# Kernel optimization log

Hardware: AMD Instinct MI355X
Metric: run time of the kernel (lower is better)

Reference implementation:

```python
import jax, jax.numpy as jnp
import numpy as np

D_MODEL = 1024
NUM_HEADS = 16
D_K = D_MODEL // NUM_HEADS
THETA = 10000.0


def setup_inputs() -> dict:
    key = jax.random.key(0)
    ks = jax.random.split(key, 5)
    b, s = 4, 1024
    std = 1.0 / np.sqrt(D_MODEL)
    x = jax.random.normal(ks[0], (b, s, D_MODEL), dtype=jnp.float32)
    token_positions = jnp.tile(jnp.arange(s, dtype=jnp.int64)[None, :], (b, 1))
    Wq = jax.random.truncated_normal(ks[1], -3.0, 3.0, (D_MODEL, D_MODEL), jnp.float32) * std
    Wk = jax.random.truncated_normal(ks[2], -3.0, 3.0, (D_MODEL, D_MODEL), jnp.float32) * std
    Wv = jax.random.truncated_normal(ks[3], -3.0, 3.0, (D_MODEL, D_MODEL), jnp.float32) * std
    Wo = jax.random.truncated_normal(ks[4], -3.0, 3.0, (D_MODEL, D_MODEL), jnp.float32) * std
    return {"x": x, "token_positions": token_positions,
            "Wq": Wq, "Wk": Wk, "Wv": Wv, "Wo": Wo}


def _apply_rope(x):
    # x: [b, h, s, d_k]; source uses row index i (ignores token_positions)
    s, d = x.shape[-2], x.shape[-1]
    pos = jnp.arange(s, dtype=jnp.float32)                      # [s]
    kidx = jnp.arange(0, d, 2, dtype=jnp.float32)               # [d/2]
    ang = pos[:, None] / (THETA ** (kidx / d))                  # [s, d/2]
    cos, sin = jnp.cos(ang), jnp.sin(ang)
    x_even, x_odd = x[..., 0::2], x[..., 1::2]                  # [b,h,s,d/2]
    out_even = x_even * cos - x_odd * sin
    out_odd = x_even * sin + x_odd * cos
    return jnp.stack([out_even, out_odd], axis=-1).reshape(x.shape)


def reference(x, token_positions, Wq, Wk, Wv, Wo):
    b, s, _ = x.shape
    # Linear: einsum '... din, dout din -> ... dout'  => x @ W.T
    q = jnp.einsum('bsd,ed->bse', x, Wq)
    k = jnp.einsum('bsd,ed->bse', x, Wk)
    v = jnp.einsum('bsd,ed->bse', x, Wv)
    # split heads -> [b, h, s, d_k]
    def split(t):
        return t.reshape(b, s, NUM_HEADS, D_K).transpose(0, 2, 1, 3)
    q, k, v = split(q), split(k), split(v)
    q = _apply_rope(q)
    k = _apply_rope(k)
    scores = jnp.einsum('bhqd,bhkd->bhqk', q, k) / np.sqrt(D_K)
    causal = jnp.tril(jnp.ones((s, s), dtype=bool))
    scores = jnp.where(causal, scores, -jnp.inf)
    attn = jax.nn.softmax(scores, axis=-1)
    out = jnp.einsum('bhqk,bhkd->bhqd', attn, v)
    out = out.transpose(0, 2, 1, 3).reshape(b, s, D_MODEL)
    return jnp.einsum('bsd,ed->bse', out, Wo)
```

## Files before the change

kernel.cpp:

```cpp
#include <hip/hip_runtime.h>

typedef __attribute__((ext_vector_type(8))) short short8;
typedef __attribute__((ext_vector_type(8))) __bf16 bf16x8;
typedef __attribute__((ext_vector_type(4))) float f32x4;
typedef __attribute__((ext_vector_type(4))) float float4v;
typedef __attribute__((ext_vector_type(4))) unsigned short ushort4v;
typedef __attribute__((ext_vector_type(2))) unsigned uint2v;
typedef __attribute__((ext_vector_type(4))) unsigned uint4v;

#define AS1 __attribute__((address_space(1)))
#define AS3 __attribute__((address_space(3)))

#define BATCH 4
#define SEQ 1024
#define DM 1024
#define NH 16
#define DKH 64
#define MROWS (BATCH * SEQ)
#define N3 (3 * DM)

static __device__ __forceinline__ unsigned short f2bf(float f) {
  unsigned u = __builtin_bit_cast(unsigned, f);
  u += 0x7FFFu + ((u >> 16) & 1u);
  return (unsigned short)(u >> 16);
}
static __device__ __forceinline__ float bf2f(unsigned short h) {
  return __builtin_bit_cast(float, ((unsigned)h) << 16);
}
static __device__ __forceinline__ unsigned cvt_pk_bf16(float lo, float hi) {
  unsigned r;
  asm("v_cvt_pk_bf16_f32 %0, %1, %2" : "=v"(r) : "v"(lo), "v"(hi));
  return r;
}
static __device__ __forceinline__ f32x4 mfma16(short8 a, short8 b, f32x4 c) {
  return __builtin_amdgcn_mfma_f32_16x16x32_bf16(
      __builtin_bit_cast(bf16x8, a), __builtin_bit_cast(bf16x8, b), c, 0, 0, 0);
}

__global__ __launch_bounds__(256) void convert_kernel(
    const float* __restrict__ x, const float* __restrict__ wq,
    const float* __restrict__ wk, const float* __restrict__ wv,
    const float* __restrict__ wo, unsigned short* __restrict__ xb,
    unsigned short* __restrict__ wqkv, unsigned short* __restrict__ wob) {
  size_t i4 = ((size_t)blockIdx.x * 256 + threadIdx.x) * 4;
  const size_t SZX = (size_t)MROWS * DM;
  const size_t SZW = (size_t)DM * DM;
  const float* src;
  unsigned short* dst;
  size_t off;
  if (i4 < SZX) {
    src = x; dst = xb; off = i4;
  } else if (i4 < SZX + SZW) {
    src = wq; dst = wqkv; off = i4 - SZX;
  } else if (i4 < SZX + 2 * SZW) {
    src = wk; dst = wqkv + SZW; off = i4 - SZX - SZW;
  } else if (i4 < SZX + 3 * SZW) {
    src = wv; dst = wqkv + 2 * SZW; off = i4 - SZX - 2 * SZW;
  } else {
    src = wo; dst = wob; off = i4 - SZX - 3 * SZW;
  }
  float4v v = *(const float4v*)(src + off);
  uint2v o;
  o.x = cvt_pk_bf16(v.x, v.y);
  o.y = cvt_pk_bf16(v.z, v.w);
  *(uint2v*)(dst + off) = o;
}

static __device__ __forceinline__ void store_c(float* p, float v) { *p = v; }
static __device__ __forceinline__ void store_c(unsigned short* p, float v) { *p = f2bf(v); }

template <typename OutT>
__global__ __launch_bounds__(256) void gemm_bt(
    const unsigned short* __restrict__ A, const unsigned short* __restrict__ B,
    OutT* __restrict__ C, int M, int N, int K) {
  __shared__ char sA[16384];
  __shared__ char sB[16384];
  const int tid = threadIdx.x, w = tid >> 6, lane = tid & 63;
  const int g = lane >> 4, r = lane & 15;
  const int m0 = blockIdx.y * 128, n0 = blockIdx.x * 128;
  const int wm = (w >> 1) * 64, wn = (w & 1) * 64;
  f32x4 acc[4][4] = {};
  for (int k0 = 0; k0 < K; k0 += 64) {
#pragma unroll
    for (int c = 0; c < 4; ++c) {
      int p = c * 4096 + tid * 16;
      int o = p ^ (((p >> 7) & 7) << 4);
      int row = o >> 7, colb = o & 127;
      const char* ga = (const char*)(A + (size_t)(m0 + row) * K + k0) + colb;
      const char* gb = (const char*)(B + (size_t)(n0 + row) * K + k0) + colb;
      __builtin_amdgcn_global_load_lds((const AS1 void*)ga,
                                       (AS3 void*)(sA + c * 4096 + (w << 10)), 16, 0, 0);
      __builtin_amdgcn_global_load_lds((const AS1 void*)gb,
                                       (AS3 void*)(sB + c * 4096 + (w << 10)), 16, 0, 0);
    }
    __syncthreads();
#pragma unroll
    for (int kk = 0; kk < 2; ++kk) {
      short8 af[4], bfr[4];
#pragma unroll
      for (int i = 0; i < 4; ++i) {
        int ra = wm + i * 16 + r;
        af[i] = *(const short8*)(sA + (((ra << 7) + (kk << 6) + (g << 4)) ^ ((ra & 7) << 4)));
        int rb = wn + i * 16 + r;
        bfr[i] = *(const short8*)(sB + (((rb << 7) + (kk << 6) + (g << 4)) ^ ((rb & 7) << 4)));
      }
#pragma unroll
      for (int i = 0; i < 4; ++i)
#pragma unroll
        for (int j = 0; j < 4; ++j) acc[i][j] = mfma16(af[i], bfr[j], acc[i][j]);
    }
    __syncthreads();
  }
#pragma unroll
  for (int i = 0; i < 4; ++i)
#pragma unroll
    for (int j = 0; j < 4; ++j)
#pragma unroll
      for (int jj = 0; jj < 4; ++jj) {
        int row = m0 + wm + i * 16 + g * 4 + jj;
        int col = n0 + wn + j * 16 + r;
        store_c(&C[(size_t)row * N + col], acc[i][j][jj]);
      }
}

__global__ __launch_bounds__(256) void gemm_n64(
    const unsigned short* __restrict__ A, const unsigned short* __restrict__ B,
    float* __restrict__ C, int M, int N, int K) {
  __shared__ char sA[16384];
  __shared__ char sB[8192];
  const int tid = threadIdx.x, w = tid >> 6, lane = tid & 63;
  const int g = lane >> 4, r = lane & 15;
  const int m0 = blockIdx.y * 128, n0 = blockIdx.x * 64;
  const int wm = (w >> 1) * 64, wn = (w & 1) * 32;
  f32x4 acc[4][2] = {};
  for (int k0 = 0; k0 < K; k0 += 64) {
#pragma unroll
    for (int c = 0; c < 4; ++c) {
      int p = c * 4096 + tid * 16;
      int o = p ^ (((p >> 7) & 7) << 4);
      int row = o >> 7, colb = o & 127;
      const char* ga = (const char*)(A + (size_t)(m0 + row) * K + k0) + colb;
      __builtin_amdgcn_global_load_lds((const AS1 void*)ga,
                                       (AS3 void*)(sA + c * 4096 + (w << 10)), 16, 0, 0);
      if (c < 2) {
        const char* gb = (const char*)(B + (size_t)(n0 + row) * K + k0) + colb;
        __builtin_amdgcn_global_load_lds((const AS1 void*)gb,
                                         (AS3 void*)(sB + c * 4096 + (w << 10)), 16, 0, 0);
      }
    }
    __syncthreads();
#pragma unroll
    for (int kk = 0; kk < 2; ++kk) {
      short8 af[4], bfr[2];
#pragma unroll
      for (int i = 0; i < 4; ++i) {
        int ra = wm + i * 16 + r;
        af[i] = *(const short8*)(sA + (((ra << 7) + (kk << 6) + (g << 4)) ^ ((ra & 7) << 4)));
      }
#pragma unroll
      for (int j = 0; j < 2; ++j) {
        int rb = wn + j * 16 + r;
        bfr[j] = *(const short8*)(sB + (((rb << 7) + (kk << 6) + (g << 4)) ^ ((rb & 7) << 4)));
      }
#pragma unroll
      for (int i = 0; i < 4; ++i)
#pragma unroll
        for (int j = 0; j < 2; ++j) acc[i][j] = mfma16(af[i], bfr[j], acc[i][j]);
    }
    __syncthreads();
  }
#pragma unroll
  for (int i = 0; i < 4; ++i)
#pragma unroll
    for (int j = 0; j < 2; ++j)
#pragma unroll
      for (int jj = 0; jj < 4; ++jj) {
        int row = m0 + wm + i * 16 + g * 4 + jj;
        int col = n0 + wn + j * 16 + r;
        C[(size_t)row * N + col] = acc[i][j][jj];
      }
}

__global__ __launch_bounds__(256) void rope_tv(const unsigned short* __restrict__ cf,
                                               unsigned short* __restrict__ qb,
                                               unsigned short* __restrict__ kb,
                                               unsigned short* __restrict__ vt) {
  __shared__ unsigned short tile[64][72];
  const int bid = blockIdx.x;
  if (bid < 2048) {
    int i = bid * 256 + threadIdx.x;
    int t8 = i & 7, h = (i >> 3) & 15, s = (i >> 7) & 1023, b = i >> 17;
    const unsigned short* src = cf + (size_t)(b * SEQ + s) * N3 + h * DKH + t8 * 8;
    short8 q8 = *(const short8*)src;
    short8 k8 = *(const short8*)(src + DM);
    uint4v qo, ko;
#pragma unroll
    for (int p = 0; p < 4; ++p) {
      int kidx = t8 * 4 + p;
      float freq = __expf(-(float)kidx * 0.28782313662425572f);
      float sn, cs;
      __sincosf((float)s * freq, &sn, &cs);
      float qe = bf2f((unsigned short)q8[2 * p]), qv = bf2f((unsigned short)q8[2 * p + 1]);
      float ke = bf2f((unsigned short)k8[2 * p]), kv = bf2f((unsigned short)k8[2 * p + 1]);
      qo[p] = cvt_pk_bf16((qe * cs - qv * sn) * 0.125f, (qe * sn + qv * cs) * 0.125f);
      ko[p] = cvt_pk_bf16(ke * cs - kv * sn, ke * sn + kv * cs);
    }
    size_t dsto = (size_t)((b * NH + h) * SEQ + s) * DKH + t8 * 8;
    *(uint4v*)(qb + dsto) = qo;
    *(uint4v*)(kb + dsto) = ko;
  } else {
    int t = bid - 2048;
    int bh = t >> 4, b = bh >> 4, h = bh & 15, s0 = (t & 15) * 64;
    int tt = threadIdx.x, row = tt >> 2, c0 = (tt & 3) * 16;
    const unsigned short* src = cf + (size_t)(b * SEQ + s0 + row) * N3 + 2 * DM + h * DKH + c0;
    short8 v0 = *(const short8*)src;
    short8 v1 = *(const short8*)(src + 8);
    *(short8*)&tile[row][c0] = v0;
    *(short8*)&tile[row][c0 + 8] = v1;
    __syncthreads();
    unsigned short* dst = vt + ((size_t)bh * DKH + row) * SEQ + s0 + c0;
    short8 o0, o1;
#pragma unroll
    for (int j = 0; j < 8; ++j) o0[j] = (short)tile[c0 + j][row];
#pragma unroll
    for (int j = 0; j < 8; ++j) o1[j] = (short)tile[c0 + 8 + j][row];
    *(short8*)dst = o0;
    *(short8*)(dst + 8) = o1;
  }
}

__global__ __launch_bounds__(256) void attn_kernel(const unsigned short* __restrict__ qb,
                                                   const unsigned short* __restrict__ kb,
                                                   const unsigned short* __restrict__ vt,
                                                   unsigned short* __restrict__ ob) {
  __shared__ char kl[2][8192];
  __shared__ char vl[2][8192];
  __shared__ unsigned short plds[4][2][1024];
  const int bx = blockIdx.x, bh = blockIdx.y, b = bh >> 4, h = bh & 15;
  const int qlo = bx, qhi = 15 - bx;
  const int tid = threadIdx.x, w = tid >> 6, lane = tid & 63;
  const int g = lane >> 4, r = lane & 15;
  const unsigned short* Q = qb + (size_t)bh * SEQ * DKH;
  const char* Kp = (const char*)(kb + (size_t)bh * SEQ * DKH);
  const char* Vp = (const char*)(vt + (size_t)bh * DKH * SEQ);

  const int p0 = (w << 10) + lane * 16;
  const int p1 = p0 + 4096;
  const int o0 = p0 ^ (((p0 >> 7) & 7) << 4);
  const int o1 = p1 ^ (((p1 >> 7) & 7) << 4);
  const int r0 = o0 >> 7, c0 = o0 & 127, r1 = o1 >> 7, c1 = o1 & 127;
  const size_t ks0 = (size_t)r0 * 128 + c0, ks1 = (size_t)r1 * 128 + c1;
  const size_t vs0 = (size_t)r0 * 2048 + c0, vs1 = (size_t)r1 * 2048 + c1;

#define STAGE_KV(bi, kt)                                                          \
  do {                                                                            \
    const char* kbase = Kp + (size_t)(kt) * 8192;                                 \
    const char* vbase = Vp + (size_t)(kt) * 128;                                  \
    __builtin_amdgcn_global_load_lds((const AS1 void*)(kbase + ks0),              \
                                     (AS3 void*)(kl[bi] + p0), 16, 0, 0);         \
    __builtin_amdgcn_global_load_lds((const AS1 void*)(kbase + ks1),              \
                                     (AS3 void*)(kl[bi] + p1), 16, 0, 0);         \
    __builtin_amdgcn_global_load_lds((const AS1 void*)(vbase + vs0),              \
                                     (AS3 void*)(vl[bi] + p0), 16, 0, 0);         \
    __builtin_amdgcn_global_load_lds((const AS1 void*)(vbase + vs1),              \
                                     (AS3 void*)(vl[bi] + p1), 16, 0, 0);         \
  } while (0)

  short8 qfL0, qfL1, qfH0, qfH1;
  {
    int qrL = qlo * 64 + w * 16 + r;
    int qrH = qhi * 64 + w * 16 + r;
    qfL0 = *(const short8*)(Q + (size_t)qrL * DKH + g * 8);
    qfL1 = *(const short8*)(Q + (size_t)qrL * DKH + 32 + g * 8);
    qfH0 = *(const short8*)(Q + (size_t)qrH * DKH + g * 8);
    qfH1 = *(const short8*)(Q + (size_t)qrH * DKH + 32 + g * 8);
  }
  f32x4 oaccL[4] = {}, oaccH[4] = {};
  float mrunL = -1e30f, lrunL = 0.f, mrunH = -1e30f, lrunH = 0.f;
  const int qgH = qhi * 64 + w * 16 + r;
  const int qgL = qlo * 64 + w * 16 + r;
  char* pbH = (char*)&plds[w][0][0];
  char* pbL = (char*)&plds[w][1][0];

  STAGE_KV(0, 0);
  __syncthreads();

  for (int kt = 0; kt <= qhi; ++kt) {
    if (kt < qhi) STAGE_KV((kt + 1) & 1, kt + 1);
    const bool doLo = (kt <= qlo);
    const char* kb_ = kl[kt & 1];
    const char* vb_ = vl[kt & 1];
    f32x4 sh[4] = {}, sl[4] = {};
#pragma unroll
    for (int nb = 0; nb < 4; ++nb) {
      int ra = nb * 16 + r;
      short8 kf0 = *(const short8*)(kb_ + ((ra * 128 + g * 16) ^ ((ra & 7) << 4)));
      short8 kf1 = *(const short8*)(kb_ + ((ra * 128 + 64 + g * 16) ^ ((ra & 7) << 4)));
      sh[nb] = mfma16(kf0, qfH0, sh[nb]);
      sh[nb] = mfma16(kf1, qfH1, sh[nb]);
      if (doLo) {
        sl[nb] = mfma16(kf0, qfL0, sl[nb]);
        sl[nb] = mfma16(kf1, qfL1, sl[nb]);
      }
    }
    if (kt == qhi) {
#pragma unroll
      for (int nb = 0; nb < 4; ++nb)
#pragma unroll
        for (int j = 0; j < 4; ++j)
          if (kt * 64 + nb * 16 + g * 4 + j > qgH) sh[nb][j] = -1e30f;
    }
    if (kt == qlo) {
#pragma unroll
      for (int nb = 0; nb < 4; ++nb)
#pragma unroll
        for (int j = 0; j < 4; ++j)
          if (kt * 64 + nb * 16 + g * 4 + j > qgL) sl[nb][j] = -1e30f;
    }
    {
      float a0 = fmaxf(fmaxf(sh[0][0], sh[0][1]), fmaxf(sh[0][2], sh[0][3]));
      float a1 = fmaxf(fmaxf(sh[1][0], sh[1][1]), fmaxf(sh[1][2], sh[1][3]));
      float a2 = fmaxf(fmaxf(sh[2][0], sh[2][1]), fmaxf(sh[2][2], sh[2][3]));
      float a3 = fmaxf(fmaxf(sh[3][0], sh[3][1]), fmaxf(sh[3][2], sh[3][3]));
      float tm = fmaxf(fmaxf(a0, a1), fmaxf(a2, a3));
      tm = fmaxf(tm, __shfl_xor(tm, 16, 64));
      tm = fmaxf(tm, __shfl_xor(tm, 32, 64));
      if (!__all(tm <= mrunH + 8.f)) {
        float mnew = fmaxf(mrunH, tm);
        float scl = __expf(mrunH - mnew);
        mrunH = mnew;
        lrunH *= scl;
#pragma unroll
        for (int db = 0; db < 4; ++db) {
          f32x4 t = oaccH[db];
          t[0] *= scl; t[1] *= scl; t[2] *= scl; t[3] *= scl;
          oaccH[db] = t;
        }
      }
      float ps = 0.f;
#pragma unroll
      for (int nb = 0; nb < 4; ++nb)
#pragma unroll
        for (int j = 0; j < 4; ++j) {
          float p = __expf(sh[nb][j] - mrunH);
          sh[nb][j] = p;
          ps += p;
        }
      ps += __shfl_xor(ps, 16, 64);
      ps += __shfl_xor(ps, 32, 64);
      lrunH += ps;
#pragma unroll
      for (int nb = 0; nb < 4; ++nb) {
        uint2v pk;
        pk.x = cvt_pk_bf16(sh[nb][0], sh[nb][1]);
        pk.y = cvt_pk_bf16(sh[nb][2], sh[nb][3]);
        *(uint2v*)(pbH + ((r * 128 + nb * 32 + g * 8) ^ ((r & 7) << 4))) = pk;
      }
    }
    if (doLo) {
      float a0 = fmaxf(fmaxf(sl[0][0], sl[0][1]), fmaxf(sl[0][2], sl[0][3]));
      float a1 = fmaxf(fmaxf(sl[1][0], sl[1][1]), fmaxf(sl[1][2], sl[1][3]));
      float a2 = fmaxf(fmaxf(sl[2][0], sl[2][1]), fmaxf(sl[2][2], sl[2][3]));
      float a3 = fmaxf(fmaxf(sl[3][0], sl[3][1]), fmaxf(sl[3][2], sl[3][3]));
      float tm = fmaxf(fmaxf(a0, a1), fmaxf(a2, a3));
      tm = fmaxf(tm, __shfl_xor(tm, 16, 64));
      tm = fmaxf(tm, __shfl_xor(tm, 32, 64));
      if (!__all(tm <= mrunL + 8.f)) {
        float mnew = fmaxf(mrunL, tm);
        float scl = __expf(mrunL - mnew);
        mrunL = mnew;
        lrunL *= scl;
#pragma unroll
        for (int db = 0; db < 4; ++db) {
          f32x4 t = oaccL[db];
          t[0] *= scl; t[1] *= scl; t[2] *= scl; t[3] *= scl;
          oaccL[db] = t;
        }
      }
      float ps = 0.f;
#pragma unroll
      for (int nb = 0; nb < 4; ++nb)
#pragma unroll
        for (int j = 0; j < 4; ++j) {
          float p = __expf(sl[nb][j] - mrunL);
          sl[nb][j] = p;
          ps += p;
        }
      ps += __shfl_xor(ps, 16, 64);
      ps += __shfl_xor(ps, 32, 64);
      lrunL += ps;
#pragma unroll
      for (int nb = 0; nb < 4; ++nb) {
        uint2v pk;
        pk.x = cvt_pk_bf16(sl[nb][0], sl[nb][1]);
        pk.y = cvt_pk_bf16(sl[nb][2], sl[nb][3]);
        *(uint2v*)(pbL + ((r * 128 + nb * 32 + g * 8) ^ ((r & 7) << 4))) = pk;
      }
    }
    asm volatile("s_waitcnt lgkmcnt(0)" ::: "memory");
    __builtin_amdgcn_sched_barrier(0);
    short8 pfH0 = *(const short8*)(pbH + ((r * 128 + g * 16) ^ ((r & 7) << 4)));
    short8 pfH1 = *(const short8*)(pbH + ((r * 128 + 64 + g * 16) ^ ((r & 7) << 4)));
    short8 pfL0, pfL1;
    if (doLo) {
      pfL0 = *(const short8*)(pbL + ((r * 128 + g * 16) ^ ((r & 7) << 4)));
      pfL1 = *(const short8*)(pbL + ((r * 128 + 64 + g * 16) ^ ((r & 7) << 4)));
    }
#pragma unroll
    for (int db = 0; db < 4; ++db) {
      int rv = db * 16 + r;
      short8 vf0 = *(const short8*)(vb_ + ((rv * 128 + g * 16) ^ ((rv & 7) << 4)));
      short8 vf1 = *(const short8*)(vb_ + ((rv * 128 + 64 + g * 16) ^ ((rv & 7) << 4)));
      oaccH[db] = mfma16(vf0, pfH0, oaccH[db]);
      oaccH[db] = mfma16(vf1, pfH1, oaccH[db]);
      if (doLo) {
        oaccL[db] = mfma16(vf0, pfL0, oaccL[db]);
        oaccL[db] = mfma16(vf1, pfL1, oaccL[db]);
      }
    }
    __syncthreads();
  }
  {
    float invH = 1.f / lrunH;
    unsigned short* orH = ob + (size_t)(b * SEQ + qgH) * DM + h * DKH;
#pragma unroll
    for (int db = 0; db < 4; ++db) {
      uint2v pk;
      pk.x = cvt_pk_bf16(oaccH[db][0] * invH, oaccH[db][1] * invH);
      pk.y = cvt_pk_bf16(oaccH[db][2] * invH, oaccH[db][3] * invH);
      *(uint2v*)(orH + db * 16 + g * 4) = pk;
    }
    float invL = 1.f / lrunL;
    unsigned short* orL = ob + (size_t)(b * SEQ + qgL) * DM + h * DKH;
#pragma unroll
    for (int db = 0; db < 4; ++db) {
      uint2v pk;
      pk.x = cvt_pk_bf16(oaccL[db][0] * invL, oaccL[db][1] * invL);
      pk.y = cvt_pk_bf16(oaccL[db][2] * invL, oaccL[db][3] * invL);
      *(uint2v*)(orL + db * 16 + g * 4) = pk;
    }
  }
#undef STAGE_KV
}

extern "C" void kernel_launch(void* const* d_in, const int* in_sizes, int n_in,
                              void* d_out, int out_size, void* d_ws, size_t ws_size,
                              hipStream_t stream) {
  const float* x = (const float*)d_in[0];
  const float* wq = (const float*)d_in[2];
  const float* wk = (const float*)d_in[3];
  const float* wv = (const float*)d_in[4];
  const float* wo = (const float*)d_in[5];
  char* ws = (char*)d_ws;
  unsigned short* xb = (unsigned short*)(ws);
  unsigned short* wqkv = (unsigned short*)(ws + (8u << 20));
  unsigned short* wob = (unsigned short*)(ws + (14u << 20));
  unsigned short* cf = (unsigned short*)(ws + (16u << 20));
  unsigned short* qbuf = (unsigned short*)(ws + (40u << 20));
  unsigned short* kbuf = (unsigned short*)(ws + (48u << 20));
  unsigned short* vtb = (unsigned short*)(ws + (56u << 20));
  unsigned short* obuf = (unsigned short*)(ws + (64u << 20));
  float* out = (float*)d_out;

  convert_kernel<<<8192, 256, 0, stream>>>(x, wq, wk, wv, wo, xb, wqkv, wob);
  gemm_bt<unsigned short><<<dim3(24, 32), 256, 0, stream>>>(xb, wqkv, cf, MROWS, N3, DM);
  rope_tv<<<3072, 256, 0, stream>>>(cf, qbuf, kbuf, vtb);
  attn_kernel<<<dim3(8, 64), 256, 0, stream>>>(qbuf, kbuf, vtb, obuf);
  gemm_n64<<<dim3(16, 32), 256, 0, stream>>>(obuf, wob, out, MROWS, DM, DM);
}
```

Before: 105.4 us.

## Vectorize GEMM epilogues, remap blocks per XCD, and use exp2 softmax

Swaps the MFMA operand order so each lane holds four consecutive columns, which lets the GEMM epilogues write packed bf16x4 or float4 stores instead of scalar stores. Block indices are remapped so that consecutive blocks on the same XCD cover neighbouring tiles, aiming for better L2 reuse. The softmax now folds log2(e) into the Q scale and uses exp2f in place of __expf, with the lazy-rescale threshold adjusted to match. Together these target store traffic, cache locality and exp instruction cost. The block remap assumes the grid dimensions divide evenly into the 8-way split.

```diff
diff --git a/kernel.cpp b/kernel.cpp
--- a/kernel.cpp
+++ b/kernel.cpp
@@ -4,7 +4,6 @@
 typedef __attribute__((ext_vector_type(8))) __bf16 bf16x8;
 typedef __attribute__((ext_vector_type(4))) float f32x4;
 typedef __attribute__((ext_vector_type(4))) float float4v;
-typedef __attribute__((ext_vector_type(4))) unsigned short ushort4v;
 typedef __attribute__((ext_vector_type(2))) unsigned uint2v;
 typedef __attribute__((ext_vector_type(4))) unsigned uint4v;
 
@@ -18,12 +17,8 @@
 #define DKH 64
 #define MROWS (BATCH * SEQ)
 #define N3 (3 * DM)
-
-static __device__ __forceinline__ unsigned short f2bf(float f) {
-  unsigned u = __builtin_bit_cast(unsigned, f);
-  u += 0x7FFFu + ((u >> 16) & 1u);
-  return (unsigned short)(u >> 16);
-}
+#define LOG2E 1.4426950408889634f
+
 static __device__ __forceinline__ float bf2f(unsigned short h) {
   return __builtin_bit_cast(float, ((unsigned)h) << 16);
 }
@@ -66,18 +61,18 @@
   *(uint2v*)(dst + off) = o;
 }
 
-static __device__ __forceinline__ void store_c(float* p, float v) { *p = v; }
-static __device__ __forceinline__ void store_c(unsigned short* p, float v) { *p = f2bf(v); }
-
-template <typename OutT>
-__global__ __launch_bounds__(256) void gemm_bt(
+__global__ __launch_bounds__(256) void gemm_qkv(
     const unsigned short* __restrict__ A, const unsigned short* __restrict__ B,
-    OutT* __restrict__ C, int M, int N, int K) {
+    unsigned short* __restrict__ C, int M, int N, int K) {
   __shared__ char sA[16384];
   __shared__ char sB[16384];
   const int tid = threadIdx.x, w = tid >> 6, lane = tid & 63;
   const int g = lane >> 4, r = lane & 15;
-  const int m0 = blockIdx.y * 128, n0 = blockIdx.x * 128;
+  const int nbx = gridDim.x, bid = blockIdx.y * nbx + blockIdx.x;
+  const int xcd = bid & 7, idx = bid >> 3, hx = nbx >> 1;
+  const int bx = (xcd & 1) * hx + idx % hx;
+  const int by = (xcd >> 1) * (gridDim.y >> 2) + idx / hx;
+  const int m0 = by * 128, n0 = bx * 128;
   const int wm = (w >> 1) * 64, wn = (w & 1) * 64;
   f32x4 acc[4][4] = {};
   for (int k0 = 0; k0 < K; k0 += 64) {
@@ -107,20 +102,21 @@
 #pragma unroll
       for (int i = 0; i < 4; ++i)
 #pragma unroll
-        for (int j = 0; j < 4; ++j) acc[i][j] = mfma16(af[i], bfr[j], acc[i][j]);
+        for (int j = 0; j < 4; ++j) acc[i][j] = mfma16(bfr[j], af[i], acc[i][j]);
     }
     __syncthreads();
   }
 #pragma unroll
   for (int i = 0; i < 4; ++i)
 #pragma unroll
-    for (int j = 0; j < 4; ++j)
-#pragma unroll
-      for (int jj = 0; jj < 4; ++jj) {
-        int row = m0 + wm + i * 16 + g * 4 + jj;
-        int col = n0 + wn + j * 16 + r;
-        store_c(&C[(size_t)row * N + col], acc[i][j][jj]);
-      }
+    for (int j = 0; j < 4; ++j) {
+      int row = m0 + wm + i * 16 + r;
+      int col = n0 + wn + j * 16 + g * 4;
+      uint2v pk;
+      pk.x = cvt_pk_bf16(acc[i][j][0], acc[i][j][1]);
+      pk.y = cvt_pk_bf16(acc[i][j][2], acc[i][j][3]);
+      *(uint2v*)(&C[(size_t)row * N + col]) = pk;
+    }
 }
 
 __global__ __launch_bounds__(256) void gemm_n64(
@@ -130,7 +126,11 @@
   __shared__ char sB[8192];
   const int tid = threadIdx.x, w = tid >> 6, lane = tid & 63;
   const int g = lane >> 4, r = lane & 15;
-  const int m0 = blockIdx.y * 128, n0 = blockIdx.x * 64;
+  const int nbx = gridDim.x, bid = blockIdx.y * nbx + blockIdx.x;
+  const int xcd = bid & 7, idx = bid >> 3, hx = nbx >> 1;
+  const int bx = (xcd & 1) * hx + idx % hx;
+  const int by = (xcd >> 1) * (gridDim.y >> 2) + idx / hx;
+  const int m0 = by * 128, n0 = bx * 64;
   const int wm = (w >> 1) * 64, wn = (w & 1) * 32;
   f32x4 acc[4][2] = {};
   for (int k0 = 0; k0 < K; k0 += 64) {
@@ -165,20 +165,18 @@
 #pragma unroll
       for (int i = 0; i < 4; ++i)
 #pragma unroll
-        for (int j = 0; j < 2; ++j) acc[i][j] = mfma16(af[i], bfr[j], acc[i][j]);
+        for (int j = 0; j < 2; ++j) acc[i][j] = mfma16(bfr[j], af[i], acc[i][j]);
     }
     __syncthreads();
   }
 #pragma unroll
   for (int i = 0; i < 4; ++i)
 #pragma unroll
-    for (int j = 0; j < 2; ++j)
-#pragma unroll
-      for (int jj = 0; jj < 4; ++jj) {
-        int row = m0 + wm + i * 16 + g * 4 + jj;
-        int col = n0 + wn + j * 16 + r;
-        C[(size_t)row * N + col] = acc[i][j][jj];
-      }
+    for (int j = 0; j < 2; ++j) {
+      int row = m0 + wm + i * 16 + r;
+      int col = n0 + wn + j * 16 + g * 4;
+      *(float4v*)(&C[(size_t)row * N + col]) = acc[i][j];
+    }
 }
 
 __global__ __launch_bounds__(256) void rope_tv(const unsigned short* __restrict__ cf,
@@ -194,6 +192,7 @@
     short8 q8 = *(const short8*)src;
     short8 k8 = *(const short8*)(src + DM);
     uint4v qo, ko;
+    const float qs = 0.125f * LOG2E;
 #pragma unroll
     for (int p = 0; p < 4; ++p) {
       int kidx = t8 * 4 + p;
@@ -202,7 +201,7 @@
       __sincosf((float)s * freq, &sn, &cs);
       float qe = bf2f((unsigned short)q8[2 * p]), qv = bf2f((unsigned short)q8[2 * p + 1]);
       float ke = bf2f((unsigned short)k8[2 * p]), kv = bf2f((unsigned short)k8[2 * p + 1]);
-      qo[p] = cvt_pk_bf16((qe * cs - qv * sn) * 0.125f, (qe * sn + qv * cs) * 0.125f);
+      qo[p] = cvt_pk_bf16((qe * cs - qv * sn) * qs, (qe * sn + qv * cs) * qs);
       ko[p] = cvt_pk_bf16(ke * cs - kv * sn, ke * sn + kv * cs);
     }
     size_t dsto = (size_t)((b * NH + h) * SEQ + s) * DKH + t8 * 8;
@@ -240,6 +239,7 @@
   const int qlo = bx, qhi = 15 - bx;
   const int tid = threadIdx.x, w = tid >> 6, lane = tid & 63;
   const int g = lane >> 4, r = lane & 15;
+  const float DEFER = 8.f * LOG2E;
   const unsigned short* Q = qb + (size_t)bh * SEQ * DKH;
   const char* Kp = (const char*)(kb + (size_t)bh * SEQ * DKH);
   const char* Vp = (const char*)(vt + (size_t)bh * DKH * SEQ);
@@ -325,9 +325,9 @@
       float tm = fmaxf(fmaxf(a0, a1), fmaxf(a2, a3));
       tm = fmaxf(tm, __shfl_xor(tm, 16, 64));
       tm = fmaxf(tm, __shfl_xor(tm, 32, 64));
-      if (!__all(tm <= mrunH + 8.f)) {
+      if (!__all(tm <= mrunH + DEFER)) {
         float mnew = fmaxf(mrunH, tm);
-        float scl = __expf(mrunH - mnew);
+        float scl = exp2f(mrunH - mnew);
         mrunH = mnew;
         lrunH *= scl;
 #pragma unroll
@@ -342,7 +342,7 @@
       for (int nb = 0; nb < 4; ++nb)
 #pragma unroll
         for (int j = 0; j < 4; ++j) {
-          float p = __expf(sh[nb][j] - mrunH);
+          float p = exp2f(sh[nb][j] - mrunH);
           sh[nb][j] = p;
           ps += p;
         }
@@ -365,9 +365,9 @@
       float tm = fmaxf(fmaxf(a0, a1), fmaxf(a2, a3));
       tm = fmaxf(tm, __shfl_xor(tm, 16, 64));
       tm = fmaxf(tm, __shfl_xor(tm, 32, 64));
-      if (!__all(tm <= mrunL + 8.f)) {
+      if (!__all(tm <= mrunL + DEFER)) {
         float mnew = fmaxf(mrunL, tm);
-        float scl = __expf(mrunL - mnew);
+        float scl = exp2f(mrunL - mnew);
         mrunL = mnew;
         lrunL *= scl;
 #pragma unroll
@@ -382,7 +382,7 @@
       for (int nb = 0; nb < 4; ++nb)
 #pragma unroll
         for (int j = 0; j < 4; ++j) {
-          float p = __expf(sl[nb][j] - mrunL);
+          float p = exp2f(sl[nb][j] - mrunL);
           sl[nb][j] = p;
           ps += p;
         }
@@ -463,7 +463,7 @@
   float* out = (float*)d_out;
 
   convert_kernel<<<8192, 256, 0, stream>>>(x, wq, wk, wv, wo, xb, wqkv, wob);
-  gemm_bt<unsigned short><<<dim3(24, 32), 256, 0, stream>>>(xb, wqkv, cf, MROWS, N3, DM);
+  gemm_qkv<<<dim3(24, 32), 256, 0, stream>>>(xb, wqkv, cf, MROWS, N3, DM);
   rope_tv<<<3072, 256, 0, stream>>>(cf, qbuf, kbuf, vtb);
   attn_kernel<<<dim3(8, 64), 256, 0, stream>>>(qbuf, kbuf, vtb, obuf);
   gemm_n64<<<dim3(16, 32), 256, 0, stream>>>(obuf, wob, out, MROWS, DM, DM);
```

Result: slower. 126.0 us (+19.5%).
